# Kernel tuning notes

Hardware: AMD Instinct MI355X
Metric: run time of the kernel (lower is better)

## Reference

```python
import jax, jax.numpy as jnp
import numpy as np

N_NODES = 100000
N_EDGES = 100000
N_MAP = 128
EPS = 1e-5


def _gn1(x, g, b):
    # GroupNorm with 1 group == per-row normalization over channels, affine per channel
    m = jnp.mean(x, axis=-1, keepdims=True)
    v = jnp.mean((x - m) ** 2, axis=-1, keepdims=True)
    return (x - m) * jax.lax.rsqrt(v + EPS) * g + b


def setup_inputs() -> dict:
    key = jax.random.key(0)
    ks = jax.random.split(key, 16)
    s = 0.02
    d = N_MAP
    inp = {
        'nodes': jax.random.normal(ks[0], (N_NODES, 8), jnp.float32),
        'indexes': jax.random.randint(ks[1], (N_EDGES, 28), 0, N_NODES, jnp.int64)
            if jax.config.jax_enable_x64 else jax.random.randint(ks[1], (N_EDGES, 28), 0, N_NODES, jnp.int32),
        'mask': jnp.full((14,), N_EDGES, dtype=jnp.int32),
        'in1_W': jax.random.normal(ks[2], (d, 2), jnp.float32) * s,
        'in1_b': jnp.zeros((d,), jnp.float32),
        'in2_W': jax.random.normal(ks[3], (d, d), jnp.float32) * s,
        'in_g': jnp.ones((d,), jnp.float32),
        'in_bg': jnp.zeros((d,), jnp.float32),
        'seg1_W': jax.random.normal(ks[4], (d, 2), jnp.float32) * s,
        'seg1_b': jnp.zeros((d,), jnp.float32),
        'seg2_W': jax.random.normal(ks[5], (d, d), jnp.float32) * s,
        'seg_g': jnp.ones((d,), jnp.float32),
        'seg_bg': jnp.zeros((d,), jnp.float32),
        'meta_W': jax.random.normal(ks[6], (d, d + 4), jnp.float32) * s,
        'meta_g': jnp.ones((d,), jnp.float32),
        'meta_bg': jnp.zeros((d,), jnp.float32),
        'ctr_W': jax.random.normal(ks[7], (4, d, d), jnp.float32) * s,
        'edge_W': jax.random.normal(ks[8], (4, 14, d, d), jnp.float32) * s,
        'norm_g': jnp.ones((4, d), jnp.float32),
        'norm_bg': jnp.zeros((4, d), jnp.float32),
        'ctr2_W': jax.random.normal(ks[9], (4, d, d), jnp.float32) * s,
        'ctr2_g': jnp.ones((4, d), jnp.float32),
        'ctr2_bg': jnp.zeros((4, d), jnp.float32),
    }
    return inp


def reference(nodes, indexes, mask, in1_W, in1_b, in2_W, in_g, in_bg,
              seg1_W, seg1_b, seg2_W, seg_g, seg_bg, meta_W, meta_g, meta_bg,
              ctr_W, edge_W, norm_g, norm_bg, ctr2_W, ctr2_g, ctr2_bg):
    relu = jax.nn.relu
    # input / seg branches: Linear+ReLU then bias-free Linear + GroupNorm(1)
    feat = _gn1(relu(nodes[:, :2] @ in1_W.T + in1_b) @ in2_W.T, in_g, in_bg)
    feat = feat + _gn1(relu(nodes[:, 2:4] @ seg1_W.T + seg1_b) @ seg2_W.T, seg_g, seg_bg)
    feat = relu(feat)
    # meta: Linear(n_map+4 -> n_map, bias-free) + GN + ReLU
    feat = relu(_gn1(jnp.concatenate([feat, nodes[:, 4:]], axis=1) @ meta_W.T, meta_g, meta_bg))
    res = feat
    E = indexes.shape[0]
    eid = jnp.arange(E)
    for i in range(4):
        temp = feat @ ctr_W[i].T
        # 14 edge types in column order: pre0..pre5, right, suc0..suc5, left
        for t in range(14):
            valid = (eid < mask[t])[:, None]          # [E,1]
            src = jnp.where(valid[:, 0], indexes[:, 2 * t + 1], 0)
            dst = jnp.where(valid[:, 0], indexes[:, 2 * t], 0)
            msg = jnp.where(valid, feat[src] @ edge_W[i, t].T, 0.0)  # [E, d]
            temp = temp.at[dst].add(msg)
        feat = relu(_gn1(temp, norm_g[i], norm_bg[i]))
        feat = _gn1(feat @ ctr2_W[i].T, ctr2_g[i], ctr2_bg[i])
        feat = relu(feat + res)
        res = feat
    return (feat, nodes[:, :2])
```

## Files before the change

### kernel.cpp

```cpp
#include <hip/hip_runtime.h>
#include <hip/hip_bf16.h>

#define NN 100000
#define NE 100000
#define NCNT (14 * NN)
#define LP 136
#define LP2 168
#define SCAN_CHUNK 4096
#define NSCB ((NCNT + SCAN_CHUNK - 1) / SCAN_CHUNK)

typedef __bf16 bf16;
typedef __bf16 bf16x8 __attribute__((ext_vector_type(8)));
typedef float  f32x4  __attribute__((ext_vector_type(4)));


__device__ __forceinline__ void gl2lds16(const bf16* g, bf16* l) {
    __builtin_amdgcn_global_load_lds(
        (const __attribute__((address_space(1))) void*)g,
        (__attribute__((address_space(3))) void*)l, 16, 0, 0);
}

__device__ __forceinline__ void zacc8(f32x4 acc[8]) {
    f32x4 z = {0.f, 0.f, 0.f, 0.f};
#pragma unroll
    for (int n = 0; n < 8; ++n) acc[n] = z;
}

__device__ __forceinline__ void gnstats(const f32x4 acc[8], float mean[4], float rs[4]) {
    float s1[4], s2[4];
#pragma unroll
    for (int r = 0; r < 4; ++r) { s1[r] = 0.f; s2[r] = 0.f; }
#pragma unroll
    for (int n = 0; n < 8; ++n)
#pragma unroll
        for (int r = 0; r < 4; ++r) { float v = acc[n][r]; s1[r] += v; s2[r] += v * v; }
#pragma unroll
    for (int off = 1; off < 16; off <<= 1) {
#pragma unroll
        for (int r = 0; r < 4; ++r) {
            s1[r] += __shfl_xor(s1[r], off, 64);
            s2[r] += __shfl_xor(s2[r], off, 64);
        }
    }
#pragma unroll
    for (int r = 0; r < 4; ++r) {
        const float m = s1[r] * 0.0078125f;
        const float v = fmaxf(s2[r] * 0.0078125f - m * m, 0.f);
        mean[r] = m;
        rs[r] = rsqrtf(v + 1e-5f);
    }
}


template<int PITCH, int COLS>
__device__ inline void stageWB(const bf16* __restrict__ Wg, bf16* Wl) {
    constexpr int NV = 128 * COLS / 8;
    for (int i = threadIdx.x; i < NV; i += 256) {
        const int e = i * 8;
        const int r = e / COLS, c = e % COLS;
        *(float4*)(&Wl[r * PITCH + c]) = ((const float4*)Wg)[i];
    }
}

template<int PITCH, int KSTEPS>
__device__ inline void mmaT(const bf16* Al, const bf16* Wl, int m0, int lane, f32x4 acc[8]) {
#pragma unroll
    for (int kk = 0; kk < KSTEPS; ++kk) {
        bf16x8 a = *(const bf16x8*)(&Al[(m0 + (lane & 15)) * PITCH + kk * 32 + (lane >> 4) * 8]);
#pragma unroll
        for (int n = 0; n < 8; ++n) {
            bf16x8 b = *(const bf16x8*)(&Wl[(n * 16 + (lane & 15)) * PITCH + kk * 32 + (lane >> 4) * 8]);
            acc[n] = __builtin_amdgcn_mfma_f32_16x16x32_bf16(a, b, acc[n], 0, 0, 0);
        }
    }
}


__device__ __forceinline__ void stageW(const bf16* __restrict__ Wg, bf16* WLbase,
                                       int w, int lane) {
#pragma unroll
    for (int k = 0; k < 4; ++k) {
        const int R = (w * 4 + k) * 4 + (lane >> 4);
        const int sg = (lane & 15) ^ ((k & 1) * 4 + (lane >> 4));
        gl2lds16(Wg + R * 128 + sg * 8, WLbase + (w * 4 + k) * 512);
    }
}

__device__ __forceinline__ void mmaW(const bf16* B, const bf16x8 afr[4],
                                     int r, int h, int r7, f32x4 acc[8]) {
#pragma unroll
    for (int kk = 0; kk < 4; ++kk) {
        const int sl = ((kk * 4 + h) ^ r7) * 8;
#pragma unroll
        for (int n = 0; n < 8; ++n) {
            const bf16x8 b = *(const bf16x8*)(B + (n * 16 + r) * 128 + sl);
            acc[n] = __builtin_amdgcn_mfma_f32_16x16x32_bf16(afr[kk], b, acc[n], 0, 0, 0);
        }
    }
}

__device__ __forceinline__ void accum_row(const bf16* __restrict__ rp, float ag[4][8]) {
    const bf16x8* q = (const bf16x8*)rp;
    bf16x8 v0 = q[0], v1 = q[4], v2 = q[8], v3 = q[12];
#pragma unroll
    for (int e = 0; e < 8; ++e) {
        ag[0][e] += (float)v0[e];
        ag[1][e] += (float)v1[e];
        ag[2][e] += (float)v2[e];
        ag[3][e] += (float)v3[e];
    }
}


__global__ void k_cvt(const float* __restrict__ s, bf16* __restrict__ d, int n) {
    for (int i = blockIdx.x * 256 + threadIdx.x; i < n; i += gridDim.x * 256)
        d[i] = (bf16)s[i];
}

__global__ void k_cvt_meta(const float* __restrict__ s, bf16* __restrict__ d) {
    for (int i = blockIdx.x * 256 + threadIdx.x; i < 128 * 160; i += gridDim.x * 256) {
        const int r = i / 160, c = i % 160;
        d[i] = (bf16)(c < 132 ? s[r * 132 + c] : 0.f);
    }
}


__global__ __launch_bounds__(256) void k_count(const int* __restrict__ idx,
                                               const int* __restrict__ mask,
                                               int* __restrict__ cnt) {
    __shared__ int lim[14];
    if (threadIdx.x < 14) lim[threadIdx.x] = min(mask[threadIdx.x], NE);
    __syncthreads();
    for (int i = blockIdx.x * 256 + threadIdx.x; i < 14 * NE; i += gridDim.x * 256) {
        const int e = i / 14, t = i - e * 14;
        if (e < lim[t]) atomicAdd(&cnt[t * NN + idx[(size_t)e * 28 + 2 * t]], 1);
    }
}

__global__ __launch_bounds__(256) void k_scanA(const int* __restrict__ cnt,
                                               int* __restrict__ ptr,
                                               int* __restrict__ tot) {
    __shared__ int sm[256];
    const int tid = threadIdx.x;
    const int base = blockIdx.x * SCAN_CHUNK + tid * 16;
    int v[16]; int run = 0;
#pragma unroll
    for (int j = 0; j < 16; ++j) {
        const int x = (base + j < NCNT) ? cnt[base + j] : 0;
        v[j] = run; run += x;
    }
    sm[tid] = run; __syncthreads();
    for (int d = 1; d < 256; d <<= 1) {
        int t = 0;
        if (tid >= d) t = sm[tid - d];
        __syncthreads();
        sm[tid] += t;
        __syncthreads();
    }
    const int off = sm[tid] - run;
#pragma unroll
    for (int j = 0; j < 16; ++j)
        if (base + j < NCNT) ptr[base + j] = v[j] + off;
    if (tid == 255) tot[blockIdx.x] = sm[255];
}

__global__ void k_scanB(int* __restrict__ tot) {
    if (threadIdx.x == 0 && blockIdx.x == 0) {
        int acc = 0;
        for (int b = 0; b < NSCB; ++b) { const int t = tot[b]; tot[b] = acc; acc += t; }
        tot[NSCB] = acc;
    }
}

__global__ __launch_bounds__(256) void k_scanC(int* __restrict__ ptr,
                                               int* __restrict__ cursor,
                                               const int* __restrict__ tot) {
    const int base = blockIdx.x * SCAN_CHUNK;
    const int o = tot[blockIdx.x];
    for (int j = threadIdx.x; j < SCAN_CHUNK; j += 256) {
        const int i = base + j;
        if (i < NCNT) { const int p = ptr[i] + o; ptr[i] = p; cursor[i] = p; }
    }
    if (blockIdx.x == 0 && threadIdx.x == 0) ptr[NCNT] = tot[NSCB];
}

__global__ __launch_bounds__(256) void k_fill(const int* __restrict__ idx,
                                              const int* __restrict__ mask,
                                              int* __restrict__ cursor,
                                              int* __restrict__ elist) {
    __shared__ int lim[14];
    if (threadIdx.x < 14) lim[threadIdx.x] = min(mask[threadIdx.x], NE);
    __syncthreads();
    for (int i = blockIdx.x * 256 + threadIdx.x; i < 14 * NE; i += gridDim.x * 256) {
        const int e = i / 14, t = i - e * 14;
        if (e < lim[t]) {
            const int dst = idx[(size_t)e * 28 + 2 * t];
            const int pos = atomicAdd(&cursor[t * NN + dst], 1);
            elist[pos] = e;
        }
    }
}

__global__ __launch_bounds__(256) void k_sortseg(const int* __restrict__ ptr,
                                                 int* __restrict__ elist,
                                                 const int* __restrict__ idx) {
    for (int i = blockIdx.x * 256 + threadIdx.x; i < NCNT; i += gridDim.x * 256) {
        const int s = ptr[i], e2 = ptr[i + 1];
        for (int a = s + 1; a < e2; ++a) {
            const int key = elist[a];
            int b = a - 1;
            while (b >= s && elist[b] > key) { elist[b + 1] = elist[b]; --b; }
            elist[b + 1] = key;
        }
        const int t = i / NN;
        for (int j = s; j < e2; ++j)
            elist[j] = idx[(size_t)elist[j] * 28 + 2 * t + 1];
    }
}


__global__ __launch_bounds__(256) void k_in(
    const float* __restrict__ nodes,
    const float* __restrict__ in1W, const float* __restrict__ in1b,
    const bf16* __restrict__ wIn2,
    const float* __restrict__ ing, const float* __restrict__ inbg,
    const float* __restrict__ seg1W, const float* __restrict__ seg1b,
    const bf16* __restrict__ wSeg2,
    const float* __restrict__ segg, const float* __restrict__ segbg,
    bf16* __restrict__ outPre)
{
    __shared__ __align__(16) bf16 Wl[128 * LP];
    __shared__ __align__(16) bf16 Al[64 * LP];
    __shared__ float w0[128], w1[128], bb[128];
    __shared__ float xs[64][4];
    const int tid = threadIdx.x;
    const int row0 = blockIdx.x * 64;
    if (tid < 64) {
        const int row = row0 + tid;
        float4 x = {0.f, 0.f, 0.f, 0.f};
        if (row < NN) x = *(const float4*)(nodes + (size_t)row * 8);
        xs[tid][0] = x.x; xs[tid][1] = x.y; xs[tid][2] = x.z; xs[tid][3] = x.w;
    }
    if (tid < 128) { w0[tid] = in1W[tid * 2]; w1[tid] = in1W[tid * 2 + 1]; bb[tid] = in1b[tid]; }
    stageWB<LP, 128>(wIn2, Wl);
    __syncthreads();
    for (int i = tid; i < 64 * 128; i += 256) {
        const int r = i >> 7, j = i & 127;
        Al[r * LP + j] = (bf16)fmaxf(xs[r][0] * w0[j] + xs[r][1] * w1[j] + bb[j], 0.f);
    }
    __syncthreads();
    const int lane = tid & 63, m0 = (tid >> 6) * 16;
    f32x4 accP[8]; zacc8(accP);
    mmaT<LP, 4>(Al, Wl, m0, lane, accP);
    __syncthreads();
    if (tid < 128) { w0[tid] = seg1W[tid * 2]; w1[tid] = seg1W[tid * 2 + 1]; bb[tid] = seg1b[tid]; }
    stageWB<LP, 128>(wSeg2, Wl);
    __syncthreads();
    for (int i = tid; i < 64 * 128; i += 256) {
        const int r = i >> 7, j = i & 127;
        Al[r * LP + j] = (bf16)fmaxf(xs[r][2] * w0[j] + xs[r][3] * w1[j] + bb[j], 0.f);
    }
    __syncthreads();
    f32x4 accQ[8]; zacc8(accQ);
    mmaT<LP, 4>(Al, Wl, m0, lane, accQ);

    float mP[4], rP[4], mQ[4], rQ[4];
    gnstats(accP, mP, rP);
    gnstats(accQ, mQ, rQ);
    float gP[8], bP[8], gQ[8], bQ[8];
#pragma unroll
    for (int n = 0; n < 8; ++n) {
        const int c = n * 16 + (lane & 15);
        gP[n] = ing[c]; bP[n] = inbg[c]; gQ[n] = segg[c]; bQ[n] = segbg[c];
    }
#pragma unroll
    for (int r = 0; r < 4; ++r) {
        const int row = row0 + m0 + (lane >> 4) * 4 + r;
        if (row < NN) {
#pragma unroll
            for (int n = 0; n < 8; ++n) {
                const float yp = (accP[n][r] - mP[r]) * rP[r] * gP[n] + bP[n];
                const float yq = (accQ[n][r] - mQ[r]) * rQ[r] * gQ[n] + bQ[n];
                outPre[(size_t)row * 128 + n * 16 + (lane & 15)] = (bf16)fmaxf(yp + yq, 0.f);
            }
        }
    }
}


__global__ __launch_bounds__(256) void k_meta(
    const bf16* __restrict__ Apre, const float* __restrict__ nodes,
    const bf16* __restrict__ Wg,
    const float* __restrict__ g, const float* __restrict__ bg,
    float* __restrict__ featF, bf16* __restrict__ featB)
{
    __shared__ __align__(16) bf16 Wl[128 * LP2];
    __shared__ __align__(16) bf16 Al[64 * LP2];
    const int row0 = blockIdx.x * 64;
    stageWB<LP2, 160>(Wg, Wl);
    {
        const int r = threadIdx.x >> 2, q = threadIdx.x & 3;
        float4* d = (float4*)(&Al[r * LP2 + q * 32]);
        const int row = row0 + r;
        if (row < NN) {
            const float4* s = (const float4*)(Apre + (size_t)row * 128 + q * 32);
            float4 a0 = s[0], a1 = s[1], a2 = s[2], a3 = s[3];
            d[0] = a0; d[1] = a1; d[2] = a2; d[3] = a3;
        } else {
            float4 z = {0.f, 0.f, 0.f, 0.f};
            d[0] = z; d[1] = z; d[2] = z; d[3] = z;
        }
    }
    if (threadIdx.x < 64) {
        const int rr = threadIdx.x, row = row0 + rr;
        bf16* d = &Al[rr * LP2 + 128];
        if (row < NN) {
            const float4 x = *(const float4*)(nodes + (size_t)row * 8 + 4);
            d[0] = (bf16)x.x; d[1] = (bf16)x.y; d[2] = (bf16)x.z; d[3] = (bf16)x.w;
        } else {
            d[0] = (bf16)0.f; d[1] = (bf16)0.f; d[2] = (bf16)0.f; d[3] = (bf16)0.f;
        }
#pragma unroll
        for (int c = 4; c < 32; ++c) d[c] = (bf16)0.f;
    }
    __syncthreads();
    const int lane = threadIdx.x & 63, m0 = (threadIdx.x >> 6) * 16;
    f32x4 acc[8]; zacc8(acc);
    mmaT<LP2, 5>(Al, Wl, m0, lane, acc);

    float mean[4], rs[4];
    gnstats(acc, mean, rs);
    float gv[8], bv[8];
#pragma unroll
    for (int n = 0; n < 8; ++n) { const int c = n * 16 + (lane & 15); gv[n] = g[c]; bv[n] = bg[c]; }
#pragma unroll
    for (int r = 0; r < 4; ++r) {
        const int row = row0 + m0 + (lane >> 4) * 4 + r;
        if (row < NN) {
            const size_t off = (size_t)row * 128 + (lane & 15);
#pragma unroll
            for (int n = 0; n < 8; ++n) {
                const float y = (acc[n][r] - mean[r]) * rs[r] * gv[n] + bv[n];
                const float o = fmaxf(y, 0.f);
                featF[off + n * 16] = o;
                featB[off + n * 16] = (bf16)o;
            }
        }
    }
}


__global__ __launch_bounds__(512, 4) void k_round(
    const bf16* __restrict__ feat,
    const int* __restrict__ ptr,
    const int* __restrict__ slist,
    const bf16* __restrict__ wEdgeR,
    const bf16* __restrict__ wCtrR,
    const bf16* __restrict__ wCtr2R,
    const float* __restrict__ ng, const float* __restrict__ nbg,
    const float* __restrict__ c2g, const float* __restrict__ c2bg,
    float* __restrict__ featF,
    bf16* __restrict__ featOut,
    float* __restrict__ outF,
    int last)
{
    __shared__ __align__(16) bf16 WL[2 * 16384];
    const int tid = threadIdx.x;
    const int w = tid >> 6, lane = tid & 63;
    const int r = lane & 15, h = lane >> 4, r7 = r & 7;
    const int m0 = w * 16;
    const int row0 = blockIdx.x * 128;
    const int grow = row0 + m0 + r;
    const bool rowok = grow < NN;

    stageW(wEdgeR, WL, w, lane);

    int p0 = 0, p1 = 0;
    if (rowok) { p0 = ptr[grow]; p1 = ptr[grow + 1]; }
    int sA = slist[p1 > p0 ? p0 : 0];

    f32x4 acc[8]; zacc8(acc);

    for (int t = 0; t < 15; ++t) {
        float ag[4][8];
#pragma unroll
        for (int kk = 0; kk < 4; ++kk)
#pragma unroll
            for (int e = 0; e < 8; ++e) ag[kk][e] = 0.f;

        if (t < 14) {
            if (rowok && p1 > p0) {
                accum_row(feat + (size_t)sA * 128 + h * 8, ag);
                for (int j = p0 + 1; j < p1; ++j)
                    accum_row(feat + (size_t)slist[j] * 128 + h * 8, ag);
            }
        } else if (rowok) {
            accum_row(feat + (size_t)grow * 128 + h * 8, ag);
        }

        if (t < 13) {
            int q0 = 0, q1 = 0;
            if (rowok) {
                const size_t i2 = (size_t)(t + 1) * NN + grow;
                q0 = ptr[i2]; q1 = ptr[i2 + 1];
            }
            const int sN = slist[q1 > q0 ? q0 : 0];
            p0 = q0; p1 = q1; sA = sN;
        }

        bf16x8 afr[4];
#pragma unroll
        for (int kk = 0; kk < 4; ++kk)
#pragma unroll
            for (int e = 0; e < 8; ++e) afr[kk][e] = (bf16)ag[kk][e];

        asm volatile("s_waitcnt vmcnt(0)" ::: "memory");
        __builtin_amdgcn_s_barrier();
        __builtin_amdgcn_sched_barrier(0);
        if (t < 13)       stageW(wEdgeR + (size_t)(t + 1) * 16384, WL + ((t + 1) & 1) * 16384, w, lane);
        else if (t == 13) stageW(wCtrR,  WL,          w, lane);
        else              stageW(wCtr2R, WL + 16384,  w, lane);
        __builtin_amdgcn_sched_barrier(0);
        mmaW(WL + (t & 1) * 16384, afr, r, h, r7, acc);
    }

    float mean[4], rsv[4];
    gnstats(acc, mean, rsv);
    float gv[8], bv[8];
#pragma unroll
    for (int n = 0; n < 8; ++n) { const int c = n * 16 + r; gv[n] = ng[c]; bv[n] = nbg[c]; }
    asm volatile("s_waitcnt vmcnt(0)" ::: "memory");
    __builtin_amdgcn_s_barrier();
    __builtin_amdgcn_sched_barrier(0);
#pragma unroll
    for (int r2 = 0; r2 < 4; ++r2) {
        const int lrow = m0 + h * 4 + r2;
#pragma unroll
        for (int n = 0; n < 8; ++n) {
            const float y = (acc[n][r2] - mean[r2]) * rsv[r2] * gv[n] + bv[n];
            const int col = n * 16 + r;
            const int slot = (col >> 3) ^ (lrow & 7);
            *(bf16*)((char*)WL + lrow * 256 + slot * 16 + (col & 7) * 2) = (bf16)fmaxf(y, 0.f);
        }
    }
    asm volatile("s_waitcnt lgkmcnt(0)" ::: "memory");
    __builtin_amdgcn_s_barrier();
    __builtin_amdgcn_sched_barrier(0);

    bf16x8 afr2[4];
    {
        const int arow = m0 + r;
#pragma unroll
        for (int kk = 0; kk < 4; ++kk) {
            const int slot = (kk * 4 + h) ^ (arow & 7);
            afr2[kk] = *(const bf16x8*)((const char*)WL + arow * 256 + slot * 16);
        }
    }
    zacc8(acc);
    mmaW(WL + 16384, afr2, r, h, r7, acc);

    gnstats(acc, mean, rsv);
#pragma unroll
    for (int n = 0; n < 8; ++n) { const int c = n * 16 + r; gv[n] = c2g[c]; bv[n] = c2bg[c]; }
#pragma unroll
    for (int r2 = 0; r2 < 4; ++r2) {
        const int orow = row0 + m0 + h * 4 + r2;
        if (orow < NN) {
            const size_t off = (size_t)orow * 128 + r;
#pragma unroll
            for (int n = 0; n < 8; ++n) {
                const float y = (acc[n][r2] - mean[r2]) * rsv[r2] * gv[n] + bv[n];
                const float o = fmaxf(y + featF[off + n * 16], 0.f);
                if (last) {
                    outF[off + n * 16] = o;
                } else {
                    featF[off + n * 16] = o;
                    featOut[off + n * 16] = (bf16)o;
                }
            }
        }
    }
}


__global__ void k_nodes(const float* __restrict__ nodes, float* __restrict__ out) {
    const int j = blockIdx.x * 256 + threadIdx.x;
    if (j < 2 * NN) out[(size_t)NN * 128 + j] = nodes[(size_t)(j >> 1) * 8 + (j & 1)];
}


extern "C" void kernel_launch(void* const* d_in, const int* in_sizes, int n_in,
                              void* d_out, int out_size, void* d_ws, size_t ws_size,
                              hipStream_t stream) {
    const float* nodes  = (const float*)d_in[0];
    const int*   idx    = (const int*)d_in[1];
    const int*   mask   = (const int*)d_in[2];
    const float* in1W   = (const float*)d_in[3];
    const float* in1b   = (const float*)d_in[4];
    const float* in2W   = (const float*)d_in[5];
    const float* ing    = (const float*)d_in[6];
    const float* inbg   = (const float*)d_in[7];
    const float* seg1W  = (const float*)d_in[8];
    const float* seg1b  = (const float*)d_in[9];
    const float* seg2W  = (const float*)d_in[10];
    const float* segg   = (const float*)d_in[11];
    const float* segbg  = (const float*)d_in[12];
    const float* metaW  = (const float*)d_in[13];
    const float* metag  = (const float*)d_in[14];
    const float* metabg = (const float*)d_in[15];
    const float* ctrW   = (const float*)d_in[16];
    const float* edgeW  = (const float*)d_in[17];
    const float* normg  = (const float*)d_in[18];
    const float* normbg = (const float*)d_in[19];
    const float* ctr2W  = (const float*)d_in[20];
    const float* ctr2g  = (const float*)d_in[21];
    const float* ctr2bg = (const float*)d_in[22];
    float* out = (float*)d_out;

    char* w = (char*)d_ws;
    float* featF  = (float*)w; w += (size_t)NN * 128 * 4;
    bf16*  featB0 = (bf16*)w;  w += (size_t)NN * 128 * 2;
    bf16*  featB1 = (bf16*)w;  w += (size_t)NN * 128 * 2;
    bf16*  preB   = (bf16*)w;  w += (size_t)NN * 128 * 2;
    bf16*  wIn2   = (bf16*)w;  w += 16384 * 2;
    bf16*  wSeg2  = (bf16*)w;  w += 16384 * 2;
    bf16*  wMeta  = (bf16*)w;  w += 20480 * 2;
    bf16*  wCtr   = (bf16*)w;  w += 65536 * 2;
    bf16*  wCtr2  = (bf16*)w;  w += 65536 * 2;
    bf16*  wEdge  = (bf16*)w;  w += (size_t)917504 * 2;
    int*   cnt    = (int*)w;   w += (size_t)NCNT * 4;
    int*   ptr    = (int*)w;   w += ((size_t)NCNT + 4) * 4;
    int*   cursor = (int*)w;   w += (size_t)NCNT * 4;
    int*   elist  = (int*)w;   w += (size_t)14 * NE * 4;
    int*   tot    = (int*)w;   w += (NSCB + 1) * 4;

    dim3 blk(256);
    const int gRows = (NN + 63) / 64;

    hipMemsetAsync(cnt, 0, (size_t)NCNT * 4, stream);
    k_count<<<2048, blk, 0, stream>>>(idx, mask, cnt);
    k_scanA<<<NSCB, blk, 0, stream>>>(cnt, ptr, tot);
    k_scanB<<<1, 64, 0, stream>>>(tot);
    k_scanC<<<NSCB, blk, 0, stream>>>(ptr, cursor, tot);
    k_fill<<<2048, blk, 0, stream>>>(idx, mask, cursor, elist);
    k_sortseg<<<2048, blk, 0, stream>>>(ptr, elist, idx);

    k_cvt<<<64, blk, 0, stream>>>(in2W, wIn2, 16384);
    k_cvt<<<64, blk, 0, stream>>>(seg2W, wSeg2, 16384);
    k_cvt_meta<<<80, blk, 0, stream>>>(metaW, wMeta);
    k_cvt<<<256, blk, 0, stream>>>(ctrW, wCtr, 65536);
    k_cvt<<<256, blk, 0, stream>>>(ctr2W, wCtr2, 65536);
    k_cvt<<<2048, blk, 0, stream>>>(edgeW, wEdge, 917504);

    k_in<<<gRows, blk, 0, stream>>>(nodes, in1W, in1b, wIn2, ing, inbg,
                                    seg1W, seg1b, wSeg2, segg, segbg, preB);
    k_meta<<<gRows, blk, 0, stream>>>(preB, nodes, wMeta, metag, metabg, featF, featB0);

    bf16* bufs[2] = { featB0, featB1 };
    const int gR2 = (NN + 127) / 128;
    for (int i = 0; i < 4; ++i) {
        k_round<<<gR2, dim3(512), 0, stream>>>(bufs[i & 1], ptr, elist,
                                               wEdge + (size_t)i * 14 * 16384,
                                               wCtr + (size_t)i * 16384,
                                               wCtr2 + (size_t)i * 16384,
                                               normg + i * 128, normbg + i * 128,
                                               ctr2g + i * 128, ctr2bg + i * 128,
                                               featF, bufs[(i + 1) & 1], out,
                                               i == 3 ? 1 : 0);
    }
    k_nodes<<<(2 * NN + 255) / 256, blk, 0, stream>>>(nodes, out);
}
```

Before: 1.074 ms.

## Prefetch neighbor indices, pack edge lists, drop fp32 residual, merge conversions

Packs (edge id, src) into 64-bit keys so sorting carries the src and no gather pass is needed. k_round now prefetches up to four source indices two edge types ahead and overlaps row loads with accumulation, which shortens the gather latency chain. It also removes the fp32 feature buffer and reads the residual from the bf16 features, which cuts memory traffic but lowers residual precision. The six weight-conversion launches are merged into one kernel.

```diff
diff --git a/kernel.cpp b/kernel.cpp
--- a/kernel.cpp
+++ b/kernel.cpp
@@ -12,6 +12,7 @@
 typedef __bf16 bf16;
 typedef __bf16 bf16x8 __attribute__((ext_vector_type(8)));
 typedef float  f32x4  __attribute__((ext_vector_type(4)));
+typedef unsigned long long u64;
 
 
 __device__ __forceinline__ void gl2lds16(const bf16* g, bf16* l) {
@@ -99,28 +100,45 @@
     }
 }
 
-__device__ __forceinline__ void accum_row(const bf16* __restrict__ rp, float ag[4][8]) {
-    const bf16x8* q = (const bf16x8*)rp;
-    bf16x8 v0 = q[0], v1 = q[4], v2 = q[8], v3 = q[12];
-#pragma unroll
-    for (int e = 0; e < 8; ++e) {
-        ag[0][e] += (float)v0[e];
-        ag[1][e] += (float)v1[e];
-        ag[2][e] += (float)v2[e];
-        ag[3][e] += (float)v3[e];
-    }
-}
-
-
-__global__ void k_cvt(const float* __restrict__ s, bf16* __restrict__ d, int n) {
-    for (int i = blockIdx.x * 256 + threadIdx.x; i < n; i += gridDim.x * 256)
-        d[i] = (bf16)s[i];
-}
-
-__global__ void k_cvt_meta(const float* __restrict__ s, bf16* __restrict__ d) {
-    for (int i = blockIdx.x * 256 + threadIdx.x; i < 128 * 160; i += gridDim.x * 256) {
-        const int r = i / 160, c = i % 160;
-        d[i] = (bf16)(c < 132 ? s[r * 132 + c] : 0.f);
+__device__ __forceinline__ void loadrow(bf16x8 e[4], const bf16* __restrict__ feat,
+                                        int s, int h) {
+    const bf16x8* q = (const bf16x8*)(feat + (size_t)s * 128 + h * 8);
+    e[0] = q[0]; e[1] = q[4]; e[2] = q[8]; e[3] = q[12];
+}
+
+__device__ __forceinline__ void faccum(float ag[4][8], const bf16x8 e[4]) {
+#pragma unroll
+    for (int kk = 0; kk < 4; ++kk)
+#pragma unroll
+        for (int j = 0; j < 8; ++j) ag[kk][j] += (float)e[kk][j];
+}
+
+
+__global__ __launch_bounds__(256) void k_cvt_all(
+    const float* __restrict__ in2W, const float* __restrict__ seg2W,
+    const float* __restrict__ metaW, const float* __restrict__ ctrW,
+    const float* __restrict__ ctr2W, const float* __restrict__ edgeW,
+    bf16* __restrict__ wIn2, bf16* __restrict__ wSeg2, bf16* __restrict__ wMeta,
+    bf16* __restrict__ wCtr, bf16* __restrict__ wCtr2, bf16* __restrict__ wEdge)
+{
+    const int total = 16384 + 16384 + 20480 + 65536 + 65536 + 917504;
+    for (int i = blockIdx.x * 256 + threadIdx.x; i < total; i += gridDim.x * 256) {
+        int j = i;
+        if (j < 16384) { wIn2[j] = (bf16)in2W[j]; continue; }
+        j -= 16384;
+        if (j < 16384) { wSeg2[j] = (bf16)seg2W[j]; continue; }
+        j -= 16384;
+        if (j < 20480) {
+            const int r = j / 160, c = j % 160;
+            wMeta[j] = (bf16)(c < 132 ? metaW[r * 132 + c] : 0.f);
+            continue;
+        }
+        j -= 20480;
+        if (j < 65536) { wCtr[j] = (bf16)ctrW[j]; continue; }
+        j -= 65536;
+        if (j < 65536) { wCtr2[j] = (bf16)ctr2W[j]; continue; }
+        j -= 65536;
+        wEdge[j] = (bf16)edgeW[j];
     }
 }
 
@@ -187,7 +205,7 @@
 __global__ __launch_bounds__(256) void k_fill(const int* __restrict__ idx,
                                               const int* __restrict__ mask,
                                               int* __restrict__ cursor,
-                                              int* __restrict__ elist) {
+                                              u64* __restrict__ el) {
     __shared__ int lim[14];
     if (threadIdx.x < 14) lim[threadIdx.x] = min(mask[threadIdx.x], NE);
     __syncthreads();
@@ -195,26 +213,23 @@
         const int e = i / 14, t = i - e * 14;
         if (e < lim[t]) {
             const int dst = idx[(size_t)e * 28 + 2 * t];
+            const int src = idx[(size_t)e * 28 + 2 * t + 1];
             const int pos = atomicAdd(&cursor[t * NN + dst], 1);
-            elist[pos] = e;
+            el[pos] = ((u64)(unsigned)e << 32) | (unsigned)src;
         }
     }
 }
 
 __global__ __launch_bounds__(256) void k_sortseg(const int* __restrict__ ptr,
-                                                 int* __restrict__ elist,
-                                                 const int* __restrict__ idx) {
+                                                 u64* __restrict__ el) {
     for (int i = blockIdx.x * 256 + threadIdx.x; i < NCNT; i += gridDim.x * 256) {
         const int s = ptr[i], e2 = ptr[i + 1];
         for (int a = s + 1; a < e2; ++a) {
-            const int key = elist[a];
+            const u64 key = el[a];
             int b = a - 1;
-            while (b >= s && elist[b] > key) { elist[b + 1] = elist[b]; --b; }
-            elist[b + 1] = key;
-        }
-        const int t = i / NN;
-        for (int j = s; j < e2; ++j)
-            elist[j] = idx[(size_t)elist[j] * 28 + 2 * t + 1];
+            while (b >= s && el[b] > key) { el[b + 1] = el[b]; --b; }
+            el[b + 1] = key;
+        }
     }
 }
 
@@ -292,7 +307,7 @@
     const bf16* __restrict__ Apre, const float* __restrict__ nodes,
     const bf16* __restrict__ Wg,
     const float* __restrict__ g, const float* __restrict__ bg,
-    float* __restrict__ featF, bf16* __restrict__ featB)
+    bf16* __restrict__ featB)
 {
     __shared__ __align__(16) bf16 Wl[128 * LP2];
     __shared__ __align__(16) bf16 Al[64 * LP2];
@@ -341,9 +356,7 @@
 #pragma unroll
             for (int n = 0; n < 8; ++n) {
                 const float y = (acc[n][r] - mean[r]) * rs[r] * gv[n] + bv[n];
-                const float o = fmaxf(y, 0.f);
-                featF[off + n * 16] = o;
-                featB[off + n * 16] = (bf16)o;
+                featB[off + n * 16] = (bf16)fmaxf(y, 0.f);
             }
         }
     }
@@ -353,13 +366,12 @@
 __global__ __launch_bounds__(512, 4) void k_round(
     const bf16* __restrict__ feat,
     const int* __restrict__ ptr,
-    const int* __restrict__ slist,
+    const int* __restrict__ sl32,
     const bf16* __restrict__ wEdgeR,
     const bf16* __restrict__ wCtrR,
     const bf16* __restrict__ wCtr2R,
     const float* __restrict__ ng, const float* __restrict__ nbg,
     const float* __restrict__ c2g, const float* __restrict__ c2bg,
-    float* __restrict__ featF,
     bf16* __restrict__ featOut,
     float* __restrict__ outF,
     int last)
@@ -377,42 +389,69 @@
 
     int p0 = 0, p1 = 0;
     if (rowok) { p0 = ptr[grow]; p1 = ptr[grow + 1]; }
-    int sA = slist[p1 > p0 ? p0 : 0];
+    int s0 = 0, s1 = 0, s2 = 0, s3 = 0;
+    {
+        const int d = p1 - p0;
+        if (d > 0) s0 = sl32[2 * p0];
+        if (d > 1) s1 = sl32[2 * (p0 + 1)];
+        if (d > 2) s2 = sl32[2 * (p0 + 2)];
+        if (d > 3) s3 = sl32[2 * (p0 + 3)];
+    }
+    int n0 = 0, n1 = 0;
+    if (rowok) { n0 = ptr[NN + grow]; n1 = ptr[NN + grow + 1]; }
 
     f32x4 acc[8]; zacc8(acc);
 
     for (int t = 0; t < 15; ++t) {
-        float ag[4][8];
-#pragma unroll
-        for (int kk = 0; kk < 4; ++kk)
-#pragma unroll
-            for (int e = 0; e < 8; ++e) ag[kk][e] = 0.f;
-
+        bf16x8 afr[4];
         if (t < 14) {
-            if (rowok && p1 > p0) {
-                accum_row(feat + (size_t)sA * 128 + h * 8, ag);
-                for (int j = p0 + 1; j < p1; ++j)
-                    accum_row(feat + (size_t)slist[j] * 128 + h * 8, ag);
+            const int d = p1 - p0;
+            bf16x8 e0[4], e1[4];
+            if (d > 0) loadrow(e0, feat, s0, h);
+            if (d > 1) loadrow(e1, feat, s1, h);
+            int u0 = 0, u1 = 0, u2 = 0, u3 = 0;
+            if (t < 13) {
+                const int dn = n1 - n0;
+                if (dn > 0) u0 = sl32[2 * n0];
+                if (dn > 1) u1 = sl32[2 * (n0 + 1)];
+                if (dn > 2) u2 = sl32[2 * (n0 + 2)];
+                if (dn > 3) u3 = sl32[2 * (n0 + 3)];
             }
-        } else if (rowok) {
-            accum_row(feat + (size_t)grow * 128 + h * 8, ag);
-        }
-
-        if (t < 13) {
             int q0 = 0, q1 = 0;
-            if (rowok) {
-                const size_t i2 = (size_t)(t + 1) * NN + grow;
-                q0 = ptr[i2]; q1 = ptr[i2 + 1];
+            if (t < 12 && rowok) {
+                const size_t b2 = (size_t)(t + 2) * NN + grow;
+                q0 = ptr[b2]; q1 = ptr[b2 + 1];
             }
-            const int sN = slist[q1 > q0 ? q0 : 0];
-            p0 = q0; p1 = q1; sA = sN;
-        }
-
-        bf16x8 afr[4];
-#pragma unroll
-        for (int kk = 0; kk < 4; ++kk)
-#pragma unroll
-            for (int e = 0; e < 8; ++e) afr[kk][e] = (bf16)ag[kk][e];
+            float ag[4][8];
+#pragma unroll
+            for (int kk = 0; kk < 4; ++kk)
+#pragma unroll
+                for (int j = 0; j < 8; ++j) ag[kk][j] = 0.f;
+            if (d > 0) faccum(ag, e0);
+            if (d > 2) loadrow(e0, feat, s2, h);
+            if (d > 1) faccum(ag, e1);
+            if (d > 3) loadrow(e1, feat, s3, h);
+            if (d > 2) faccum(ag, e0);
+            if (d > 3) faccum(ag, e1);
+            for (int j = p0 + 4; j < p1; ++j) {
+                loadrow(e0, feat, sl32[2 * j], h);
+                faccum(ag, e0);
+            }
+#pragma unroll
+            for (int kk = 0; kk < 4; ++kk)
+#pragma unroll
+                for (int j = 0; j < 8; ++j) afr[kk][j] = (bf16)ag[kk][j];
+            p0 = n0; p1 = n1;
+            s0 = u0; s1 = u1; s2 = u2; s3 = u3;
+            n0 = q0; n1 = q1;
+        } else {
+            bf16x8 e0[4];
+            if (rowok) loadrow(e0, feat, grow, h);
+            else { bf16x8 z{}; e0[0] = e0[1] = e0[2] = e0[3] = z; }
+#pragma unroll
+            for (int kk = 0; kk < 4; ++kk) afr[kk] = e0[kk];
+        }
+        if (!rowok) { bf16x8 z{}; afr[0] = afr[1] = afr[2] = afr[3] = z; }
 
         asm volatile("s_waitcnt vmcnt(0)" ::: "memory");
         __builtin_amdgcn_s_barrier();
@@ -467,16 +506,15 @@
         const int orow = row0 + m0 + h * 4 + r2;
         if (orow < NN) {
             const size_t off = (size_t)orow * 128 + r;
+            float res[8];
+#pragma unroll
+            for (int n = 0; n < 8; ++n) res[n] = (float)feat[off + n * 16];
 #pragma unroll
             for (int n = 0; n < 8; ++n) {
                 const float y = (acc[n][r2] - mean[r2]) * rsv[r2] * gv[n] + bv[n];
-                const float o = fmaxf(y + featF[off + n * 16], 0.f);
-                if (last) {
-                    outF[off + n * 16] = o;
-                } else {
-                    featF[off + n * 16] = o;
-                    featOut[off + n * 16] = (bf16)o;
-                }
+                const float o = fmaxf(y + res[n], 0.f);
+                if (last) outF[off + n * 16] = o;
+                else      featOut[off + n * 16] = (bf16)o;
             }
         }
     }
@@ -518,7 +556,6 @@
     float* out = (float*)d_out;
 
     char* w = (char*)d_ws;
-    float* featF  = (float*)w; w += (size_t)NN * 128 * 4;
     bf16*  featB0 = (bf16*)w;  w += (size_t)NN * 128 * 2;
     bf16*  featB1 = (bf16*)w;  w += (size_t)NN * 128 * 2;
     bf16*  preB   = (bf16*)w;  w += (size_t)NN * 128 * 2;
@@ -531,7 +568,7 @@
     int*   cnt    = (int*)w;   w += (size_t)NCNT * 4;
     int*   ptr    = (int*)w;   w += ((size_t)NCNT + 4) * 4;
     int*   cursor = (int*)w;   w += (size_t)NCNT * 4;
-    int*   elist  = (int*)w;   w += (size_t)14 * NE * 4;
+    u64*   elist  = (u64*)w;   w += (size_t)14 * NE * 8 + 64;
     int*   tot    = (int*)w;   w += (NSCB + 1) * 4;
 
     dim3 blk(256);
@@ -543,29 +580,25 @@
     k_scanB<<<1, 64, 0, stream>>>(tot);
     k_scanC<<<NSCB, blk, 0, stream>>>(ptr, cursor, tot);
     k_fill<<<2048, blk, 0, stream>>>(idx, mask, cursor, elist);
-    k_sortseg<<<2048, blk, 0, stream>>>(ptr, elist, idx);
-
-    k_cvt<<<64, blk, 0, stream>>>(in2W, wIn2, 16384);
-    k_cvt<<<64, blk, 0, stream>>>(seg2W, wSeg2, 16384);
-    k_cvt_meta<<<80, blk, 0, stream>>>(metaW, wMeta);
-    k_cvt<<<256, blk, 0, stream>>>(ctrW, wCtr, 65536);
-    k_cvt<<<256, blk, 0, stream>>>(ctr2W, wCtr2, 65536);
-    k_cvt<<<2048, blk, 0, stream>>>(edgeW, wEdge, 917504);
+    k_sortseg<<<2048, blk, 0, stream>>>(ptr, elist);
+
+    k_cvt_all<<<1024, blk, 0, stream>>>(in2W, seg2W, metaW, ctrW, ctr2W, edgeW,
+                                        wIn2, wSeg2, wMeta, wCtr, wCtr2, wEdge);
 
     k_in<<<gRows, blk, 0, stream>>>(nodes, in1W, in1b, wIn2, ing, inbg,
                                     seg1W, seg1b, wSeg2, segg, segbg, preB);
-    k_meta<<<gRows, blk, 0, stream>>>(preB, nodes, wMeta, metag, metabg, featF, featB0);
+    k_meta<<<gRows, blk, 0, stream>>>(preB, nodes, wMeta, metag, metabg, featB0);
 
     bf16* bufs[2] = { featB0, featB1 };
     const int gR2 = (NN + 127) / 128;
     for (int i = 0; i < 4; ++i) {
-        k_round<<<gR2, dim3(512), 0, stream>>>(bufs[i & 1], ptr, elist,
+        k_round<<<gR2, dim3(512), 0, stream>>>(bufs[i & 1], ptr, (const int*)elist,
                                                wEdge + (size_t)i * 14 * 16384,
                                                wCtr + (size_t)i * 16384,
                                                wCtr2 + (size_t)i * 16384,
                                                normg + i * 128, normbg + i * 128,
                                                ctr2g + i * 128, ctr2bg + i * 128,
-                                               featF, bufs[(i + 1) & 1], out,
+                                               bufs[(i + 1) & 1], out,
                                                i == 3 ? 1 : 0);
     }
     k_nodes<<<(2 * NN + 255) / 256, blk, 0, stream>>>(nodes, out);
```

Result: slower. 1.491 ms (+38.9%).
